# Kernel tuning notes

Measured on AMD Instinct MI355X. Metric: run time of the kernel, lower is better.

Reference implementation:

```python
import jax, jax.numpy as jnp
import numpy as np

ATT_DIM = 768
N_HEADS = 4
N_LABELS = 2000
NEG_INF = -1e6


def setup_inputs() -> dict:
    key = jax.random.key(0)
    k1, k2, k3, k4, k5, k6 = jax.random.split(key, 6)
    B, S, D = 4, 3072, ATT_DIM
    h = jax.random.normal(k1, (B, S, D), dtype=jnp.float32)
    attention_mask = jnp.ones((B, S), dtype=jnp.int32)
    label_feat = jax.random.normal(k2, (N_LABELS * N_HEADS, D), dtype=jnp.float32)
    # nn.Linear W: weight [D, D], bias [D]
    W_w = jax.random.normal(k3, (D, D), dtype=jnp.float32) * 0.02
    W_b = jnp.zeros((D,), dtype=jnp.float32)
    # classifier: weight [num_labels, D], bias [num_labels]
    cls_w = jax.random.normal(k4, (N_LABELS, D), dtype=jnp.float32) * 0.02
    cls_b = jnp.zeros((N_LABELS,), dtype=jnp.float32)
    return {"h": h, "attention_mask": attention_mask, "label_feat": label_feat,
            "W_w": W_w, "W_b": W_b, "cls_w": cls_w, "cls_b": cls_b}


def reference(h, attention_mask, label_feat, W_w, W_b, cls_w, cls_b):
    # h: [B,S,D]; label_feat: [E*H, D]
    B, S, D = h.shape
    E = label_feat.shape[0] // N_HEADS
    z = jnp.tanh(h @ W_w.T + W_b)                       # [B,S,D]
    u = label_feat.reshape(E, N_HEADS, D)               # [E,H,D]
    # score 'abd,ecd->aebc' -> [B,E,S,H]
    score = jnp.einsum('bsd,ehd->besh', z, u)
    mask = attention_mask.astype(bool)[:, None, :, None]  # [B,1,S,1]
    score = jnp.where(mask, score, NEG_INF)
    alpha = jax.nn.softmax(score, axis=2)               # softmax over seq
    # m 'abd,aebc->aedc' -> [B,E,D,H]
    m = jnp.einsum('bsd,besh->bedh', h, alpha)
    m = m.max(axis=-1)                                  # head max-pool -> [B,E,D]
    logits = jnp.sum(cls_w[None] * m, axis=2) + cls_b   # [B,E]
    return logits, m
```

## Files before the change

### kernel.cpp

```cpp
#include <hip/hip_runtime.h>
#include <hip/hip_bf16.h>

typedef _Float16 f16;
typedef _Float16 half8 __attribute__((ext_vector_type(8)));
typedef _Float16 half4v __attribute__((ext_vector_type(4)));
typedef float f32x4 __attribute__((ext_vector_type(4)));

#define B_ 4
#define S_ 3072
#define D_ 768
#define E_ 2000
#define NEG_INF -1.0e6f

#define GLD16(gsrc, ldst)                                                     \
  __builtin_amdgcn_global_load_lds(                                           \
      (const __attribute__((address_space(1))) void*)(gsrc),                  \
      (__attribute__((address_space(3))) void*)(ldst), 16, 0, 0)

__global__ __launch_bounds__(256) void k_transpose(const float* __restrict__ h,
                                                   f16* __restrict__ ht) {
  __shared__ f16 tile[64][65];
  int b = blockIdx.z, s0 = blockIdx.x * 64, d0 = blockIdx.y * 64;
  int t = threadIdx.x, tx = t & 63, ty = t >> 6;
  const float* src = h + ((size_t)b * S_ + s0) * D_ + d0;
#pragma unroll
  for (int i = 0; i < 16; ++i) {
    int sl = i * 4 + ty;
    tile[sl][tx] = (f16)src[(size_t)sl * D_ + tx];
  }
  __syncthreads();
  f16* dst = ht + ((size_t)b * D_ + d0) * S_ + s0;
#pragma unroll
  for (int i = 0; i < 16; ++i) {
    int dl = i * 4 + ty;
    dst[(size_t)dl * S_ + tx] = tile[tx][dl];
  }
}

__global__ __launch_bounds__(256) void k_zgemm(const float* __restrict__ h,
                                               const float* __restrict__ W,
                                               const float* __restrict__ bias,
                                               f16* __restrict__ zb) {
  __shared__ f16 As[64][40];
  __shared__ f16 Bs[64][40];
  int i0 = blockIdx.x * 64, j0 = blockIdx.y * 64;
  int t = threadIdx.x, w = t >> 6, lane = t & 63, g = lane >> 4, li = lane & 15;
  int wi = w >> 1, wj = w & 1;

  f32x4 acc[2][2];
#pragma unroll
  for (int a = 0; a < 2; ++a)
#pragma unroll
    for (int b2 = 0; b2 < 2; ++b2) acc[a][b2] = (f32x4){0.f, 0.f, 0.f, 0.f};

  int srow = t >> 2, scol = (t & 3) * 8;
  const float* pA = h + (size_t)(i0 + srow) * D_ + scol;
  const float* pB = W + (size_t)(j0 + srow) * D_ + scol;

  for (int kc = 0; kc < D_; kc += 32) {
    float4 a0 = *(const float4*)(pA + kc);
    float4 a1 = *(const float4*)(pA + kc + 4);
    float4 b0 = *(const float4*)(pB + kc);
    float4 b1 = *(const float4*)(pB + kc + 4);
    half8 av = {(f16)a0.x, (f16)a0.y, (f16)a0.z, (f16)a0.w,
                (f16)a1.x, (f16)a1.y, (f16)a1.z, (f16)a1.w};
    half8 bv = {(f16)b0.x, (f16)b0.y, (f16)b0.z, (f16)b0.w,
                (f16)b1.x, (f16)b1.y, (f16)b1.z, (f16)b1.w};
    *(half8*)&As[srow][scol] = av;
    *(half8*)&Bs[srow][scol] = bv;
    __syncthreads();
#pragma unroll
    for (int it = 0; it < 2; ++it) {
      half8 af = *(const half8*)&As[wi * 32 + it * 16 + li][g * 8];
#pragma unroll
      for (int jt = 0; jt < 2; ++jt) {
        half8 bf = *(const half8*)&Bs[wj * 32 + jt * 16 + li][g * 8];
        acc[it][jt] =
            __builtin_amdgcn_mfma_f32_16x16x32_f16(af, bf, acc[it][jt], 0, 0, 0);
      }
    }
    __syncthreads();
  }
#pragma unroll
  for (int it = 0; it < 2; ++it) {
#pragma unroll
    for (int jt = 0; jt < 2; ++jt) {
      int jj = j0 + wj * 32 + jt * 16 + li;
      float bsv = bias[jj];
#pragma unroll
      for (int r = 0; r < 4; ++r) {
        int ii = i0 + wi * 32 + it * 16 + g * 4 + r;
        float v = acc[it][jt][r] + bsv;
        zb[(size_t)ii * D_ + jj] = (f16)tanhf(v);
      }
    }
  }
}

__global__ __launch_bounds__(512)
__attribute__((amdgpu_waves_per_eu(2, 2)))
void k_attn(const float* __restrict__ lf,
            const f16* __restrict__ zb,
            const f16* __restrict__ ht,
            const int* __restrict__ amask,
            float* __restrict__ out_m) {
  __shared__ f16 KsBuf[2][32 * 768];
  __shared__ f16 VsBuf[768 * 32];
  __shared__ f16 PtBuf[64 * 32];
  __shared__ float Cp[32][68];
  __shared__ float Fac[64];
  __shared__ float Lfin[64];
  __shared__ int Msk[2][32];

  char* KsB = (char*)&KsBuf[0][0];
  char* VsB = (char*)VsBuf;
  char* PtB = (char*)PtBuf;

  const int fid = blockIdx.x;
  const int x2 = fid & 7, u = fid >> 3;
  const int b = x2 >> 1;
  const int qtile = (x2 & 1) * 64 + u;
  if (qtile >= 125) return;
  const int q0 = qtile * 64;

  const int t = threadIdx.x, w = t >> 6, lane = t & 63;
  const int g = lane >> 4, li = lane & 15;
  const int qt = w & 3, kh = w >> 2;
  const int dh = w;

  half8 qf[12];
  {
    const float* qp = lf + (size_t)(q0 + qt * 16 + li) * D_ + kh * 384 + g * 8;
#pragma unroll
    for (int f = 0; f < 12; ++f) {
      float4 v0 = *(const float4*)(qp + f * 32);
      float4 v1 = *(const float4*)(qp + f * 32 + 4);
      qf[f] = (half8){(f16)v0.x, (f16)v0.y, (f16)v0.z, (f16)v0.w,
                      (f16)v1.x, (f16)v1.y, (f16)v1.z, (f16)v1.w};
    }
  }

  int klds[6], kgsw[6];
#pragma unroll
  for (int k = 0; k < 6; ++k) {
    int lin = (w * 6 + k) * 1024 + lane * 16;
    int row = lin / 1536;
    int xo = lin - row * 1536;
    klds[k] = lin;
    kgsw[k] = row * 1536 + (xo ^ ((row & 7) << 4));
  }
  int vlds[6], vgsw[6];
#pragma unroll
  for (int k = 0; k < 6; ++k) {
    int j = w * 6 + k;
    int vd = j * 16 + (lane >> 2);
    vlds[k] = j * 1024 + lane * 16;
    vgsw[k] = vd * (S_ * 2) + (((lane & 3) * 16) ^ ((vd & 3) << 4));
  }

  const int amask7 = (li & 7) << 4;
  const int arow0 = li * 1536 + kh * 768;
  const int arow1 = (16 + li) * 1536 + kh * 768;

  const int vroff = (dh * 96 + li) * 64 + ((g * 16) ^ ((li & 3) << 4));
  int ptoff[4];
#pragma unroll
  for (int qs = 0; qs < 4; ++qs)
    ptoff[qs] = (qs * 16 + li) * 64 + ((g * 16) ^ ((li & 3) << 4));

  const int pwoff0 = (qt * 16 + li) * 64 + ((g * 8) ^ ((li & 3) << 4));
  const int pwoff1 = (qt * 16 + li) * 64 + ((32 + g * 8) ^ ((li & 3) << 4));

  const char* zbB = (const char*)zb + (size_t)b * S_ * 1536;
  const char* htB = (const char*)ht + (size_t)b * D_ * S_ * 2;

#pragma unroll
  for (int k = 0; k < 6; ++k) GLD16(zbB + kgsw[k], KsB + klds[k]);
  if (t < 32) Msk[0][t] = amask[b * S_ + t];
  asm volatile("s_waitcnt vmcnt(0)" ::: "memory");
  __syncthreads();

  float mreg = -3.0e38f, lreg = 0.0f;
  f32x4 oacc[4][6];
#pragma unroll
  for (int a = 0; a < 4; ++a)
#pragma unroll
    for (int d = 0; d < 6; ++d) oacc[a][d] = (f32x4){0.f, 0.f, 0.f, 0.f};

  for (int i = 0; i < 96; ++i) {
    const int s0 = i * 32;
    const int s0n = (i < 95) ? s0 + 32 : 0;
    const int cur = i & 1, nxt = cur ^ 1;
    const char* ksC = KsB + cur * 49152;

    int mnext = (t < 32) ? amask[b * S_ + s0n + t] : 0;
    {
      const char* src = htB + (size_t)s0 * 2;
#pragma unroll
      for (int k = 0; k < 6; ++k) GLD16(src + vgsw[k], VsB + vlds[k]);
    }

    f32x4 c0 = {0.f, 0.f, 0.f, 0.f}, c1 = {0.f, 0.f, 0.f, 0.f};
    f32x4 e0 = {0.f, 0.f, 0.f, 0.f}, e1 = {0.f, 0.f, 0.f, 0.f};
    __builtin_amdgcn_s_setprio(1);
#pragma unroll
    for (int kf = 0; kf < 6; ++kf) {
      const int col = (kf * 64 + g * 16) ^ amask7;
      half8 a0 = *(const half8*)(ksC + arow0 + col);
      half8 a1 = *(const half8*)(ksC + arow1 + col);
      c0 = __builtin_amdgcn_mfma_f32_16x16x32_f16(a0, qf[kf], c0, 0, 0, 0);
      c1 = __builtin_amdgcn_mfma_f32_16x16x32_f16(a1, qf[kf], c1, 0, 0, 0);
    }
#pragma unroll
    for (int kf = 6; kf < 12; ++kf) {
      const int col = (kf * 64 + g * 16) ^ amask7;
      half8 a0 = *(const half8*)(ksC + arow0 + col);
      half8 a1 = *(const half8*)(ksC + arow1 + col);
      e0 = __builtin_amdgcn_mfma_f32_16x16x32_f16(a0, qf[kf], e0, 0, 0, 0);
      e1 = __builtin_amdgcn_mfma_f32_16x16x32_f16(a1, qf[kf], e1, 0, 0, 0);
    }
    __builtin_amdgcn_s_setprio(0);
    c0 = c0 + e0;
    c1 = c1 + e1;

    __builtin_amdgcn_sched_barrier(0);
    {
      const char* src = zbB + (size_t)s0n * 1536;
      char* dst = KsB + nxt * 49152;
#pragma unroll
      for (int k = 0; k < 6; ++k) GLD16(src + kgsw[k], dst + klds[k]);
    }

    if (kh == 1) {
#pragma unroll
      for (int r = 0; r < 4; ++r) {
        Cp[g * 4 + r][qt * 16 + li] = c0[r];
        Cp[16 + g * 4 + r][qt * 16 + li] = c1[r];
      }
    }
    asm volatile("s_waitcnt lgkmcnt(0)" ::: "memory");
    __builtin_amdgcn_s_barrier();

    if (kh == 0) {
      const int* mk = Msk[i & 1];
      float p[8];
      float vmax = -3.0e38f;
#pragma unroll
      for (int r = 0; r < 4; ++r) {
        float sv0 = c0[r] + Cp[g * 4 + r][qt * 16 + li];
        float sv1 = c1[r] + Cp[16 + g * 4 + r][qt * 16 + li];
        if (!mk[g * 4 + r]) sv0 = NEG_INF;
        if (!mk[16 + g * 4 + r]) sv1 = NEG_INF;
        p[r] = sv0;
        p[4 + r] = sv1;
        vmax = fmaxf(vmax, fmaxf(sv0, sv1));
      }
      vmax = fmaxf(vmax, __shfl_xor(vmax, 16));
      vmax = fmaxf(vmax, __shfl_xor(vmax, 32));
      float Mn = fmaxf(mreg, vmax);
      float fec = __expf(mreg - Mn);
      mreg = Mn;
      float ts = 0.f;
#pragma unroll
      for (int r = 0; r < 8; ++r) {
        p[r] = __expf(p[r] - Mn);
        ts += p[r];
      }
      ts += __shfl_xor(ts, 16);
      ts += __shfl_xor(ts, 32);
      lreg = lreg * fec + ts;
      if (lane < 16) Fac[qt * 16 + li] = fec;
      *(half4v*)(PtB + pwoff0) =
          (half4v){(f16)p[0], (f16)p[1], (f16)p[2], (f16)p[3]};
      *(half4v*)(PtB + pwoff1) =
          (half4v){(f16)p[4], (f16)p[5], (f16)p[6], (f16)p[7]};
    }
    if (t < 32) Msk[(i + 1) & 1][t] = mnext;
    asm volatile("s_waitcnt vmcnt(6) lgkmcnt(0)" ::: "memory");
    __builtin_amdgcn_s_barrier();

    {
      float fr[4][4];
#pragma unroll
      for (int qs = 0; qs < 4; ++qs)
#pragma unroll
        for (int r = 0; r < 4; ++r) fr[qs][r] = Fac[qs * 16 + g * 4 + r];
#pragma unroll
      for (int qs = 0; qs < 4; ++qs)
#pragma unroll
        for (int dt = 0; dt < 6; ++dt)
#pragma unroll
          for (int r = 0; r < 4; ++r) oacc[qs][dt][r] *= fr[qs][r];
      half8 pa[4];
#pragma unroll
      for (int qs = 0; qs < 4; ++qs) pa[qs] = *(const half8*)(PtB + ptoff[qs]);
      __builtin_amdgcn_s_setprio(1);
#pragma unroll
      for (int dt = 0; dt < 6; ++dt) {
        half8 vb = *(const half8*)(VsB + vroff + dt * 1024);
#pragma unroll
        for (int qs = 0; qs < 4; ++qs)
          oacc[qs][dt] =
              __builtin_amdgcn_mfma_f32_16x16x32_f16(pa[qs], vb, oacc[qs][dt], 0, 0, 0);
      }
      __builtin_amdgcn_s_setprio(0);
    }
    asm volatile("s_waitcnt vmcnt(0)" ::: "memory");
    __builtin_amdgcn_s_barrier();
  }

  if (kh == 0 && lane < 16) Lfin[qt * 16 + li] = lreg;
  __syncthreads();

#pragma unroll
  for (int qs = 0; qs < 4; ++qs) {
    float rl[4];
#pragma unroll
    for (int r = 0; r < 4; ++r) rl[r] = 1.0f / Lfin[qs * 16 + g * 4 + r];
    int e_loc = qs * 4 + g;
    float* od = out_m + ((size_t)b * E_ + (q0 >> 2) + e_loc) * D_ + dh * 96 + li;
#pragma unroll
    for (int dt = 0; dt < 6; ++dt) {
      float mv = oacc[qs][dt][0] * rl[0];
      mv = fmaxf(mv, oacc[qs][dt][1] * rl[1]);
      mv = fmaxf(mv, oacc[qs][dt][2] * rl[2]);
      mv = fmaxf(mv, oacc[qs][dt][3] * rl[3]);
      od[dt * 16] = mv;
    }
  }
}

__global__ __launch_bounds__(256) void k_logits(const float* __restrict__ cw,
                                                const float* __restrict__ cb,
                                                const float* __restrict__ m,
                                                float* __restrict__ out) {
  int t = threadIdx.x, w = t >> 6, lane = t & 63;
  int rid = blockIdx.x * 4 + w;
  int b = rid / E_, e = rid - b * E_;
  const float* mr = m + (size_t)rid * D_;
  const float* cr = cw + (size_t)e * D_;
  float acc = 0.f;
#pragma unroll
  for (int i = 0; i < 12; ++i) acc += cr[i * 64 + lane] * mr[i * 64 + lane];
#pragma unroll
  for (int off = 32; off >= 1; off >>= 1) acc += __shfl_xor(acc, off);
  if (lane == 0) out[rid] = acc + cb[e];
}

extern "C" void kernel_launch(void* const* d_in, const int* in_sizes, int n_in,
                              void* d_out, int out_size, void* d_ws, size_t ws_size,
                              hipStream_t stream) {
  const float* h = (const float*)d_in[0];
  const int* amask = (const int*)d_in[1];
  const float* lf = (const float*)d_in[2];
  const float* Ww = (const float*)d_in[3];
  const float* Wb = (const float*)d_in[4];
  const float* cw = (const float*)d_in[5];
  const float* cb = (const float*)d_in[6];
  float* out = (float*)d_out;

  f16* zb = (f16*)d_ws;
  f16* ht = (f16*)((char*)d_ws + 18874368);

  k_transpose<<<dim3(48, 12, 4), 256, 0, stream>>>(h, ht);
  k_zgemm<<<dim3(192, 12), 256, 0, stream>>>(h, Ww, Wb, zb);
  k_attn<<<512, 512, 0, stream>>>(lf, zb, ht, amask, out + 8000);
  k_logits<<<2000, 256, 0, stream>>>(cw, cb, out + 8000, out);
}
```

Measured before the change: 614.3 us.

## Switch attention kernel to 32x32x16 MFMA with 4-way K-split score reduction

```diff
diff --git a/kernel.cpp b/kernel.cpp
--- a/kernel.cpp
+++ b/kernel.cpp
@@ -5,6 +5,7 @@
 typedef _Float16 half8 __attribute__((ext_vector_type(8)));
 typedef _Float16 half4v __attribute__((ext_vector_type(4)));
 typedef float f32x4 __attribute__((ext_vector_type(4)));
+typedef float f32x16 __attribute__((ext_vector_type(16)));
 
 #define B_ 4
 #define S_ 3072
@@ -104,17 +105,14 @@
             const f16* __restrict__ ht,
             const int* __restrict__ amask,
             float* __restrict__ out_m) {
-  __shared__ f16 KsBuf[2][32 * 768];
-  __shared__ f16 VsBuf[768 * 32];
-  __shared__ f16 PtBuf[64 * 32];
-  __shared__ float Cp[32][68];
-  __shared__ float Fac[64];
-  __shared__ float Lfin[64];
-  __shared__ int Msk[2][32];
-
-  char* KsB = (char*)&KsBuf[0][0];
-  char* VsB = (char*)VsBuf;
-  char* PtB = (char*)PtBuf;
+  __shared__ __align__(16) char Lds[160256];
+  char* KsB = Lds;
+  char* VsB = Lds + 98304;
+  char* CpB = Lds + 147456;
+  char* PtB = CpB + 8192;
+  float* FacB = (float*)(Lds + 159744);
+  int* MskI = (int*)(Lds + 160000);
+  float* LfinB = (float*)(Lds + 160000);
 
   const int fid = blockIdx.x;
   const int x2 = fid & 7, u = fid >> 3;
@@ -122,28 +120,29 @@
   const int qtile = (x2 & 1) * 64 + u;
   if (qtile >= 125) return;
   const int q0 = qtile * 64;
-
-  const int t = threadIdx.x, w = t >> 6, lane = t & 63;
-  const int g = lane >> 4, li = lane & 15;
-  const int qt = w & 3, kh = w >> 2;
+  const int e0 = qtile * 16;
+
+  const int t = threadIdx.x, w = t >> 6, l = t & 63;
+  const int l31 = l & 31, h = l >> 5, h16 = h * 16;
+  const int qh = w & 1, kq = w >> 1;
   const int dh = w;
 
   half8 qf[12];
   {
-    const float* qp = lf + (size_t)(q0 + qt * 16 + li) * D_ + kh * 384 + g * 8;
-#pragma unroll
-    for (int f = 0; f < 12; ++f) {
-      float4 v0 = *(const float4*)(qp + f * 32);
-      float4 v1 = *(const float4*)(qp + f * 32 + 4);
-      qf[f] = (half8){(f16)v0.x, (f16)v0.y, (f16)v0.z, (f16)v0.w,
-                      (f16)v1.x, (f16)v1.y, (f16)v1.z, (f16)v1.w};
+    const float* qp = lf + (size_t)(q0 + qh * 32 + l31) * D_ + kq * 192 + h * 8;
+#pragma unroll
+    for (int kf = 0; kf < 12; ++kf) {
+      float4 v0 = *(const float4*)(qp + kf * 16);
+      float4 v1 = *(const float4*)(qp + kf * 16 + 4);
+      qf[kf] = (half8){(f16)v0.x, (f16)v0.y, (f16)v0.z, (f16)v0.w,
+                       (f16)v1.x, (f16)v1.y, (f16)v1.z, (f16)v1.w};
     }
   }
 
   int klds[6], kgsw[6];
 #pragma unroll
   for (int k = 0; k < 6; ++k) {
-    int lin = (w * 6 + k) * 1024 + lane * 16;
+    int lin = (w * 6 + k) * 1024 + l * 16;
     int row = lin / 1536;
     int xo = lin - row * 1536;
     klds[k] = lin;
@@ -153,181 +152,199 @@
 #pragma unroll
   for (int k = 0; k < 6; ++k) {
     int j = w * 6 + k;
-    int vd = j * 16 + (lane >> 2);
-    vlds[k] = j * 1024 + lane * 16;
-    vgsw[k] = vd * (S_ * 2) + (((lane & 3) * 16) ^ ((vd & 3) << 4));
-  }
-
-  const int amask7 = (li & 7) << 4;
-  const int arow0 = li * 1536 + kh * 768;
-  const int arow1 = (16 + li) * 1536 + kh * 768;
-
-  const int vroff = (dh * 96 + li) * 64 + ((g * 16) ^ ((li & 3) << 4));
-  int ptoff[4];
-#pragma unroll
-  for (int qs = 0; qs < 4; ++qs)
-    ptoff[qs] = (qs * 16 + li) * 64 + ((g * 16) ^ ((li & 3) << 4));
-
-  const int pwoff0 = (qt * 16 + li) * 64 + ((g * 8) ^ ((li & 3) << 4));
-  const int pwoff1 = (qt * 16 + li) * 64 + ((32 + g * 8) ^ ((li & 3) << 4));
+    int vd = j * 16 + (l >> 2);
+    vlds[k] = j * 1024 + l * 16;
+    vgsw[k] = vd * (S_ * 2) + (((l & 3) * 16) ^ (((vd >> 1) & 3) << 4));
+  }
+
+  const int am7 = (l & 7) << 4;
+  const int abase = l31 * 1536 + kq * 384;
+
+  const int rswz = ((l31 >> 1) & 3) << 4;
+  const int cqoff = l31 * 64;
+  const int csl = (kq >= 1) ? ((kq - 1) * 2 + qh) : 0;
 
   const char* zbB = (const char*)zb + (size_t)b * S_ * 1536;
   const char* htB = (const char*)ht + (size_t)b * D_ * S_ * 2;
 
 #pragma unroll
   for (int k = 0; k < 6; ++k) GLD16(zbB + kgsw[k], KsB + klds[k]);
-  if (t < 32) Msk[0][t] = amask[b * S_ + t];
   asm volatile("s_waitcnt vmcnt(0)" ::: "memory");
   __syncthreads();
 
   float mreg = -3.0e38f, lreg = 0.0f;
-  f32x4 oacc[4][6];
-#pragma unroll
-  for (int a = 0; a < 4; ++a)
-#pragma unroll
-    for (int d = 0; d < 6; ++d) oacc[a][d] = (f32x4){0.f, 0.f, 0.f, 0.f};
+  f32x16 oacc[2][3];
+#pragma unroll
+  for (int a = 0; a < 2; ++a)
+#pragma unroll
+    for (int d = 0; d < 3; ++d)
+#pragma unroll
+      for (int j = 0; j < 16; ++j) oacc[a][d][j] = 0.f;
 
   for (int i = 0; i < 96; ++i) {
     const int s0 = i * 32;
     const int s0n = (i < 95) ? s0 + 32 : 0;
-    const int cur = i & 1, nxt = cur ^ 1;
-    const char* ksC = KsB + cur * 49152;
-
-    int mnext = (t < 32) ? amask[b * S_ + s0n + t] : 0;
+    const char* ksC = KsB + (i & 1) * 49152;
+    char* ksN = KsB + ((i & 1) ^ 1) * 49152;
+
+    int mcur = (t < 32) ? amask[b * S_ + s0 + t] : 0;
     {
       const char* src = htB + (size_t)s0 * 2;
 #pragma unroll
       for (int k = 0; k < 6; ++k) GLD16(src + vgsw[k], VsB + vlds[k]);
     }
-
-    f32x4 c0 = {0.f, 0.f, 0.f, 0.f}, c1 = {0.f, 0.f, 0.f, 0.f};
-    f32x4 e0 = {0.f, 0.f, 0.f, 0.f}, e1 = {0.f, 0.f, 0.f, 0.f};
+    f32x16 ca, cb2;
+#pragma unroll
+    for (int j = 0; j < 16; ++j) { ca[j] = 0.f; cb2[j] = 0.f; }
     __builtin_amdgcn_s_setprio(1);
 #pragma unroll
     for (int kf = 0; kf < 6; ++kf) {
-      const int col = (kf * 64 + g * 16) ^ amask7;
-      half8 a0 = *(const half8*)(ksC + arow0 + col);
-      half8 a1 = *(const half8*)(ksC + arow1 + col);
-      c0 = __builtin_amdgcn_mfma_f32_16x16x32_f16(a0, qf[kf], c0, 0, 0, 0);
-      c1 = __builtin_amdgcn_mfma_f32_16x16x32_f16(a1, qf[kf], c1, 0, 0, 0);
+      half8 a = *(const half8*)(ksC + abase + ((kf * 32 + h16) ^ am7));
+      ca = __builtin_amdgcn_mfma_f32_32x32x16_f16(a, qf[kf], ca, 0, 0, 0);
     }
 #pragma unroll
     for (int kf = 6; kf < 12; ++kf) {
-      const int col = (kf * 64 + g * 16) ^ amask7;
-      half8 a0 = *(const half8*)(ksC + arow0 + col);
-      half8 a1 = *(const half8*)(ksC + arow1 + col);
-      e0 = __builtin_amdgcn_mfma_f32_16x16x32_f16(a0, qf[kf], e0, 0, 0, 0);
-      e1 = __builtin_amdgcn_mfma_f32_16x16x32_f16(a1, qf[kf], e1, 0, 0, 0);
+      half8 a = *(const half8*)(ksC + abase + ((kf * 32 + h16) ^ am7));
+      cb2 = __builtin_amdgcn_mfma_f32_32x32x16_f16(a, qf[kf], cb2, 0, 0, 0);
     }
     __builtin_amdgcn_s_setprio(0);
-    c0 = c0 + e0;
-    c1 = c1 + e1;
+#pragma unroll
+    for (int j = 0; j < 16; ++j) ca[j] += cb2[j];
 
     __builtin_amdgcn_sched_barrier(0);
     {
       const char* src = zbB + (size_t)s0n * 1536;
-      char* dst = KsB + nxt * 49152;
-#pragma unroll
-      for (int k = 0; k < 6; ++k) GLD16(src + kgsw[k], dst + klds[k]);
-    }
-
-    if (kh == 1) {
-#pragma unroll
-      for (int r = 0; r < 4; ++r) {
-        Cp[g * 4 + r][qt * 16 + li] = c0[r];
-        Cp[16 + g * 4 + r][qt * 16 + li] = c1[r];
-      }
-    }
+#pragma unroll
+      for (int k = 0; k < 6; ++k) GLD16(src + kgsw[k], ksN + klds[k]);
+    }
+    if (kq != 0) {
+      char* cp = CpB + csl * 2048 + cqoff;
+#pragma unroll
+      for (int rr = 0; rr < 4; ++rr) {
+        half4v pk = {(f16)ca[4 * rr], (f16)ca[4 * rr + 1], (f16)ca[4 * rr + 2],
+                     (f16)ca[4 * rr + 3]};
+        *(half4v*)(cp + ((rr * 16 + h * 8) ^ rswz)) = pk;
+      }
+    }
+    asm volatile("s_waitcnt vmcnt(12)" ::: "memory");
+    if (t < 32) MskI[t] = mcur;
     asm volatile("s_waitcnt lgkmcnt(0)" ::: "memory");
     __builtin_amdgcn_s_barrier();
 
-    if (kh == 0) {
-      const int* mk = Msk[i & 1];
-      float p[8];
+    if (kq == 0) {
+#pragma unroll
+      for (int kk = 1; kk < 4; ++kk) {
+        const char* sp = CpB + ((kk - 1) * 2 + qh) * 2048 + cqoff;
+#pragma unroll
+        for (int rr = 0; rr < 4; ++rr) {
+          half4v pk = *(const half4v*)(sp + ((rr * 16 + h * 8) ^ rswz));
+          ca[4 * rr + 0] += (float)pk[0];
+          ca[4 * rr + 1] += (float)pk[1];
+          ca[4 * rr + 2] += (float)pk[2];
+          ca[4 * rr + 3] += (float)pk[3];
+        }
+      }
+      float p[16];
       float vmax = -3.0e38f;
 #pragma unroll
-      for (int r = 0; r < 4; ++r) {
-        float sv0 = c0[r] + Cp[g * 4 + r][qt * 16 + li];
-        float sv1 = c1[r] + Cp[16 + g * 4 + r][qt * 16 + li];
-        if (!mk[g * 4 + r]) sv0 = NEG_INF;
-        if (!mk[16 + g * 4 + r]) sv1 = NEG_INF;
-        p[r] = sv0;
-        p[4 + r] = sv1;
-        vmax = fmaxf(vmax, fmaxf(sv0, sv1));
-      }
-      vmax = fmaxf(vmax, __shfl_xor(vmax, 16));
+      for (int rr = 0; rr < 4; ++rr) {
+        int4 m4 = *(const int4*)(MskI + rr * 8 + h * 4);
+#pragma unroll
+        for (int j = 0; j < 4; ++j) {
+          float sv = ca[4 * rr + j];
+          if (!((&m4.x)[j])) sv = NEG_INF;
+          p[4 * rr + j] = sv;
+          vmax = fmaxf(vmax, sv);
+        }
+      }
       vmax = fmaxf(vmax, __shfl_xor(vmax, 32));
       float Mn = fmaxf(mreg, vmax);
       float fec = __expf(mreg - Mn);
       mreg = Mn;
       float ts = 0.f;
 #pragma unroll
-      for (int r = 0; r < 8; ++r) {
-        p[r] = __expf(p[r] - Mn);
-        ts += p[r];
-      }
-      ts += __shfl_xor(ts, 16);
+      for (int j = 0; j < 16; ++j) {
+        p[j] = __expf(p[j] - Mn);
+        ts += p[j];
+      }
       ts += __shfl_xor(ts, 32);
       lreg = lreg * fec + ts;
-      if (lane < 16) Fac[qt * 16 + li] = fec;
-      *(half4v*)(PtB + pwoff0) =
-          (half4v){(f16)p[0], (f16)p[1], (f16)p[2], (f16)p[3]};
-      *(half4v*)(PtB + pwoff1) =
-          (half4v){(f16)p[4], (f16)p[5], (f16)p[6], (f16)p[7]};
-    }
-    if (t < 32) Msk[(i + 1) & 1][t] = mnext;
+      if (l < 32) FacB[qh * 32 + l] = fec;
+      char* pw = PtB + qh * 2048 + cqoff;
+#pragma unroll
+      for (int rr = 0; rr < 4; ++rr) {
+        half4v pk = {(f16)p[4 * rr], (f16)p[4 * rr + 1], (f16)p[4 * rr + 2],
+                     (f16)p[4 * rr + 3]};
+        *(half4v*)(pw + ((rr * 16 + h * 8) ^ rswz)) = pk;
+      }
+    }
     asm volatile("s_waitcnt vmcnt(6) lgkmcnt(0)" ::: "memory");
     __builtin_amdgcn_s_barrier();
 
     {
-      float fr[4][4];
-#pragma unroll
-      for (int qs = 0; qs < 4; ++qs)
-#pragma unroll
-        for (int r = 0; r < 4; ++r) fr[qs][r] = Fac[qs * 16 + g * 4 + r];
-#pragma unroll
-      for (int qs = 0; qs < 4; ++qs)
-#pragma unroll
-        for (int dt = 0; dt < 6; ++dt)
-#pragma unroll
-          for (int r = 0; r < 4; ++r) oacc[qs][dt][r] *= fr[qs][r];
-      half8 pa[4];
-#pragma unroll
-      for (int qs = 0; qs < 4; ++qs) pa[qs] = *(const half8*)(PtB + ptoff[qs]);
+      f32x4 frv[2][4];
+#pragma unroll
+      for (int q2 = 0; q2 < 2; ++q2)
+#pragma unroll
+        for (int rr = 0; rr < 4; ++rr)
+          frv[q2][rr] = *(const f32x4*)(FacB + q2 * 32 + rr * 8 + h * 4);
+#pragma unroll
+      for (int q2 = 0; q2 < 2; ++q2)
+#pragma unroll
+        for (int dt = 0; dt < 3; ++dt)
+#pragma unroll
+          for (int j = 0; j < 16; ++j)
+            oacc[q2][dt][j] *= frv[q2][j >> 2][j & 3];
+      half8 pa[2][2];
+#pragma unroll
+      for (int q2 = 0; q2 < 2; ++q2)
+#pragma unroll
+        for (int ss = 0; ss < 2; ++ss)
+          pa[q2][ss] = *(const half8*)(PtB + q2 * 2048 + cqoff +
+                                       ((ss * 32 + h16) ^ rswz));
       __builtin_amdgcn_s_setprio(1);
 #pragma unroll
-      for (int dt = 0; dt < 6; ++dt) {
-        half8 vb = *(const half8*)(VsB + vroff + dt * 1024);
-#pragma unroll
-        for (int qs = 0; qs < 4; ++qs)
-          oacc[qs][dt] =
-              __builtin_amdgcn_mfma_f32_16x16x32_f16(pa[qs], vb, oacc[qs][dt], 0, 0, 0);
-      }
+      for (int dt = 0; dt < 3; ++dt)
+#pragma unroll
+        for (int ss = 0; ss < 2; ++ss) {
+          half8 vb = *(const half8*)(VsB + (dh * 96 + dt * 32 + l31) * 64 +
+                                     ((ss * 32 + h16) ^ rswz));
+#pragma unroll
+          for (int q2 = 0; q2 < 2; ++q2)
+            oacc[q2][dt] = __builtin_amdgcn_mfma_f32_32x32x16_f16(
+                pa[q2][ss], vb, oacc[q2][dt], 0, 0, 0);
+        }
       __builtin_amdgcn_s_setprio(0);
     }
     asm volatile("s_waitcnt vmcnt(0)" ::: "memory");
     __builtin_amdgcn_s_barrier();
   }
 
-  if (kh == 0 && lane < 16) Lfin[qt * 16 + li] = lreg;
+  if (kq == 0 && l < 32) LfinB[qh * 32 + l] = lreg;
   __syncthreads();
 
-#pragma unroll
-  for (int qs = 0; qs < 4; ++qs) {
-    float rl[4];
-#pragma unroll
-    for (int r = 0; r < 4; ++r) rl[r] = 1.0f / Lfin[qs * 16 + g * 4 + r];
-    int e_loc = qs * 4 + g;
-    float* od = out_m + ((size_t)b * E_ + (q0 >> 2) + e_loc) * D_ + dh * 96 + li;
-#pragma unroll
-    for (int dt = 0; dt < 6; ++dt) {
-      float mv = oacc[qs][dt][0] * rl[0];
-      mv = fmaxf(mv, oacc[qs][dt][1] * rl[1]);
-      mv = fmaxf(mv, oacc[qs][dt][2] * rl[2]);
-      mv = fmaxf(mv, oacc[qs][dt][3] * rl[3]);
-      od[dt * 16] = mv;
-    }
-  }
+  f32x4 rlv[2][4];
+#pragma unroll
+  for (int q2 = 0; q2 < 2; ++q2)
+#pragma unroll
+    for (int rr = 0; rr < 4; ++rr) {
+      f32x4 lv = *(const f32x4*)(LfinB + q2 * 32 + rr * 8 + h * 4);
+      rlv[q2][rr] =
+          (f32x4){1.0f / lv[0], 1.0f / lv[1], 1.0f / lv[2], 1.0f / lv[3]};
+    }
+#pragma unroll
+  for (int q2 = 0; q2 < 2; ++q2)
+#pragma unroll
+    for (int dt = 0; dt < 3; ++dt)
+#pragma unroll
+      for (int rr = 0; rr < 4; ++rr) {
+        float mv = oacc[q2][dt][4 * rr + 0] * rlv[q2][rr][0];
+        mv = fmaxf(mv, oacc[q2][dt][4 * rr + 1] * rlv[q2][rr][1]);
+        mv = fmaxf(mv, oacc[q2][dt][4 * rr + 2] * rlv[q2][rr][2]);
+        mv = fmaxf(mv, oacc[q2][dt][4 * rr + 3] * rlv[q2][rr][3]);
+        int e_loc = q2 * 8 + rr * 2 + h;
+        out_m[((size_t)b * E_ + e0 + e_loc) * D_ + dh * 96 + dt * 32 + l31] = mv;
+      }
 }
 
 __global__ __launch_bounds__(256) void k_logits(const float* __restrict__ cw,
```

New measurement: 779.4 us. 26.9% more time.
